# Optimization experiments

Hardware: AMD Instinct MI355X
Metric: run time of the kernel (lower is better)

## Reference

```python
import jax, jax.numpy as jnp
import numpy as np

H = 24
HEAD_DIM = 128
EPS = 1e-6
IP_SCALE = 1.0

def _rms(x, w):
    return x * jax.lax.rsqrt(jnp.mean(x * x, axis=-1, keepdims=True) + EPS) * w

def _heads(x, B):
    # (B, S, H*D) -> (B, H, S, D)
    return x.reshape(B, x.shape[1], H, HEAD_DIM).transpose(0, 2, 1, 3)

def _merge(x):
    B, h, S, d = x.shape
    return x.transpose(0, 2, 1, 3).reshape(B, S, h * d)

def _sdpa(q, k, v):
    s = jnp.einsum('bhqd,bhkd->bhqk', q, k) * (1.0 / np.sqrt(HEAD_DIM))
    return jnp.einsum('bhqk,bhkd->bhqd', jax.nn.softmax(s, axis=-1), v)

def _rope(x, cos, sin):
    # Flux-style real rotary: interleaved pairs, out = x*cos + rot(x)*sin
    xr = x.reshape(x.shape[:-1] + (-1, 2))
    x1, x2 = xr[..., 0], xr[..., 1]
    xrot = jnp.stack([-x2, x1], axis=-1).reshape(x.shape)
    return x * cos + xrot * sin

def setup_inputs():
    key = jax.random.key(0)
    ks = jax.random.split(key, 24)
    B, S_img, L_txt, D, IP_DIM, N_IP = 1, 2048, 512, 3072, 2048, 1024
    S = S_img + L_txt
    def w(k, i, o):
        return jax.random.normal(k, (i, o), jnp.float32) * 0.02
    def b(k, o):
        return jax.random.normal(k, (o,), jnp.float32) * 0.01
    pos = jnp.arange(S, dtype=jnp.float32)
    freqs = 1.0 / (10000.0 ** (jnp.arange(0, HEAD_DIM, 2, dtype=jnp.float32) / HEAD_DIM))
    ang = pos[:, None] * freqs[None, :]
    cos = jnp.repeat(jnp.cos(ang), 2, axis=-1)  # (S, HEAD_DIM)
    sin = jnp.repeat(jnp.sin(ang), 2, axis=-1)
    return {
        'hidden_states': jax.random.normal(ks[0], (B, S_img, D), jnp.float32),
        'encoder_hidden_states': jax.random.normal(ks[1], (B, L_txt, D), jnp.float32),
        'ip_hidden_states': jax.random.normal(ks[2], (B, N_IP, IP_DIM), jnp.float32),
        'rot_cos': cos, 'rot_sin': sin,
        'Wq': w(ks[3], D, D), 'bq': b(ks[4], D),
        'Wk': w(ks[5], D, D), 'bk': b(ks[6], D),
        'Wv': w(ks[7], D, D), 'bv': b(ks[8], D),
        'norm_q_w': jnp.ones((HEAD_DIM,), jnp.float32),
        'norm_k_w': jnp.ones((HEAD_DIM,), jnp.float32),
        'aWq': w(ks[9], D, D), 'abq': b(ks[10], D),
        'aWk': w(ks[11], D, D), 'abk': b(ks[12], D),
        'aWv': w(ks[13], D, D), 'abv': b(ks[14], D),
        'norm_aq_w': jnp.ones((HEAD_DIM,), jnp.float32),
        'norm_ak_w': jnp.ones((HEAD_DIM,), jnp.float32),
        'Wk_ip': w(ks[15], IP_DIM, D), 'bk_ip': b(ks[16], D),
        'Wv_ip': w(ks[17], IP_DIM, D), 'bv_ip': b(ks[18], D),
        'norm_ipq_w': jnp.ones((HEAD_DIM,), jnp.float32),
        'norm_ipk_w': jnp.ones((HEAD_DIM,), jnp.float32),
        'Wo': w(ks[19], D, D), 'bo': b(ks[20], D),
        'Wao': w(ks[21], D, D), 'bao': b(ks[22], D),
    }

def reference(hidden_states, encoder_hidden_states, ip_hidden_states, rot_cos, rot_sin,
              Wq, bq, Wk, bk, Wv, bv, norm_q_w, norm_k_w,
              aWq, abq, aWk, abk, aWv, abv, norm_aq_w, norm_ak_w,
              Wk_ip, bk_ip, Wv_ip, bv_ip, norm_ipq_w, norm_ipk_w,
              Wo, bo, Wao, bao):
    B, S_img, D = hidden_states.shape
    L = encoder_hidden_states.shape[1]
    q = _heads(hidden_states @ Wq + bq, B)   # (B,H,S_img,d)
    k = _heads(hidden_states @ Wk + bk, B)
    v = _heads(hidden_states @ Wv + bv, B)
    # IP-adapter cross-attention: RMS-normed raw image query vs projected image tokens
    ip_q = _rms(q, norm_ipq_w)
    ip_k = _rms(_heads(ip_hidden_states @ Wk_ip + bk_ip, B), norm_ipk_w)
    ip_v = _heads(ip_hidden_states @ Wv_ip + bv_ip, B)
    ip_out = _merge(_sdpa(ip_q, ip_k, ip_v))  # (B, S_img, D)
    # main joint attention with per-head QK RMSNorm
    q = _rms(q, norm_q_w)
    k = _rms(k, norm_k_w)
    eq = _rms(_heads(encoder_hidden_states @ aWq + abq, B), norm_aq_w)
    ek = _rms(_heads(encoder_hidden_states @ aWk + abk, B), norm_ak_w)
    ev = _heads(encoder_hidden_states @ aWv + abv, B)
    q = jnp.concatenate([eq, q], axis=2)
    k = jnp.concatenate([ek, k], axis=2)
    v = jnp.concatenate([ev, v], axis=2)
    q = _rope(q, rot_cos, rot_sin)
    k = _rope(k, rot_cos, rot_sin)
    hs = _merge(_sdpa(q, k, v))  # (B, L+S_img, D)
    enc = hs[:, :L]
    img = hs[:, L:] + IP_SCALE * ip_out
    img = img @ Wo + bo
    enc = enc @ Wao + bao
    return (img, enc)
```

## Files before the change

### kernel.cpp

```cpp
#include <hip/hip_runtime.h>
#include <hip/hip_bf16.h>
#include <cmath>
#include <cstdint>

#define H_    24
#define HD_   128
#define D_    3072
#define SIMG_ 2048
#define LTXT_ 512
#define SALL_ 2560
#define NIP_  1024
#define IPD_  2048

using bf16 = __hip_bfloat16;
typedef __bf16 bf16x8 __attribute__((ext_vector_type(8)));
typedef float  f32x4  __attribute__((ext_vector_type(4)));
typedef short  short8 __attribute__((ext_vector_type(8)));
typedef unsigned int uint4v __attribute__((ext_vector_type(4)));

#define QSCALE_ 0.12751741f

#define SWZ_BLOCK(bx, by)                                              \
  {                                                                    \
    int _gx = gridDim.x;                                               \
    int _hw = blockIdx.x + blockIdx.y * _gx;                           \
    int _n  = _gx * gridDim.y;                                         \
    int _lid = (_hw & 7) * (_n >> 3) + (_hw >> 3);                     \
    bx = _lid % _gx;                                                   \
    by = _lid / _gx;                                                   \
  }

__device__ __forceinline__ unsigned short f2bf(float f) {
  unsigned int u = __float_as_uint(f);
  unsigned int r = (u + 0x7fffu + ((u >> 16) & 1u)) >> 16;
  return (unsigned short)r;
}
__device__ __forceinline__ float bf2f(unsigned short u) {
  return __uint_as_float(((unsigned int)u) << 16);
}
__device__ __forceinline__ unsigned int cvtpk(float lo, float hi) {
  unsigned int pk;
  asm("v_cvt_pk_bf16_f32 %0, %1, %2" : "=v"(pk) : "v"(lo), "v"(hi));
  return pk;
}

__device__ __forceinline__ void gload16(const void* g, void* l) {
  __builtin_amdgcn_global_load_lds(
      (const __attribute__((address_space(1))) unsigned*)g,
      (__attribute__((address_space(3))) unsigned*)l, 16, 0, 0);
}


__global__ void cast_kernel(const float* __restrict__ x, unsigned short* __restrict__ y, int n4) {
  int i = blockIdx.x * blockDim.x + threadIdx.x;
  if (i >= n4) return;
  float4 v = reinterpret_cast<const float4*>(x)[i];
  ushort4 o = make_ushort4(f2bf(v.x), f2bf(v.y), f2bf(v.z), f2bf(v.w));
  reinterpret_cast<ushort4*>(y)[i] = o;
}

__global__ __launch_bounds__(512)
void transpose_cast3_kernel(const float* __restrict__ W0, const float* __restrict__ W1,
                            const float* __restrict__ W2, unsigned short* __restrict__ Wt,
                            int R, int C) {
  __shared__ float tile[64][69];
  const float* W = blockIdx.z == 0 ? W0 : (blockIdx.z == 1 ? W1 : W2);
  unsigned short* dst = Wt + (size_t)blockIdx.z * R * C;
  int bx = blockIdx.x * 64, by = blockIdx.y * 64;
  int tx = threadIdx.x, ty = threadIdx.y;
#pragma unroll
  for (int i = 0; i < 2; i++) {
    int r = ty + 32 * i;
    float4 v = *reinterpret_cast<const float4*>(&W[(size_t)(by + r) * C + bx + tx * 4]);
    tile[r][tx * 4 + 0] = v.x; tile[r][tx * 4 + 1] = v.y;
    tile[r][tx * 4 + 2] = v.z; tile[r][tx * 4 + 3] = v.w;
  }
  __syncthreads();
  int tid = ty * 16 + tx;
  int c = tid >> 3, r0 = (tid & 7) * 8;
  short8 o;
#pragma unroll
  for (int j = 0; j < 8; j++) o[j] = (short)f2bf(tile[r0 + j][c]);
  *reinterpret_cast<short8*>(&dst[(size_t)(bx + c) * R + by + r0]) = o;
}

__device__ __forceinline__ void gemm_core64(const bf16* __restrict__ Ab, const bf16* __restrict__ Bb,
                                            int K, bf16* Alds, bf16* Blds, int t,
                                            int wid, int l16, int lg, f32x4 (&acc)[2][8]) {
  char* AldsB = (char*)Alds + t * 16;
  char* BldsB = (char*)Blds + t * 16;
  for (int kt = 0; kt < K; kt += 64) {
    __syncthreads();
#pragma unroll
    for (int p = 0; p < 4; p++) {
      gload16(Ab + (size_t)(32 * p) * K + kt, AldsB + p * 4096);
      gload16(Bb + (size_t)(32 * p) * K + kt, BldsB + p * 4096);
    }
    __syncthreads();
#pragma unroll
    for (int kb = 0; kb < 2; kb++) {
      bf16x8 af[2], bfr[8];
#pragma unroll
      for (int mi = 0; mi < 2; mi++) {
        int r = wid * 32 + mi * 16 + l16;
        af[mi] = *reinterpret_cast<const bf16x8*>(
            (char*)Alds + r * 128 + ((lg * 16 + kb * 64) ^ ((r & 7) << 4)));
      }
#pragma unroll
      for (int ni = 0; ni < 8; ni++) {
        int r = ni * 16 + l16;
        bfr[ni] = *reinterpret_cast<const bf16x8*>(
            (char*)Blds + r * 128 + ((lg * 16 + kb * 64) ^ ((r & 7) << 4)));
      }
      __builtin_amdgcn_s_setprio(1);
#pragma unroll
      for (int mi = 0; mi < 2; mi++)
#pragma unroll
        for (int ni = 0; ni < 8; ni++)
          acc[mi][ni] = __builtin_amdgcn_mfma_f32_16x16x32_bf16(af[mi], bfr[ni], acc[mi][ni], 0, 0, 0);
      __builtin_amdgcn_s_setprio(0);
    }
  }
}

__global__ __launch_bounds__(256)
void gemm_proj_kernel(const bf16* __restrict__ A, const bf16* __restrict__ Wt,
                      int M, int K, int projmap,
                      const float* __restrict__ b0, const float* __restrict__ b1,
                      const float* __restrict__ b2,
                      const float* __restrict__ rcos, const float* __restrict__ rsin,
                      int pos_off, int tok_off, int Sout,
                      unsigned short* __restrict__ qa_p, const float* __restrict__ nq,
                      unsigned short* __restrict__ ipq_p, const float* __restrict__ nipq, int Sip,
                      unsigned short* __restrict__ ka_p, const float* __restrict__ nk,
                      unsigned short* __restrict__ va_p) {
  __shared__ __align__(16) bf16 Alds[128 * 64];
  __shared__ __align__(16) bf16 Blds[128 * 64];
  bf16* VtS = Alds;
  int t = threadIdx.x;
  int lane = t & 63, wid = t >> 6;
  int l16 = lane & 15, lg = lane >> 4;
  int bx, by;
  SWZ_BLOCK(bx, by);
  int bm = bx * 128;
  int proj = by / 24, head = by % 24;
  int code = (projmap >> (proj * 4)) & 15;
  int arow = t >> 3;
  int aseg = (t & 7) ^ (arow & 7);

  f32x4 acc[2][8];
#pragma unroll
  for (int i = 0; i < 2; i++)
#pragma unroll
    for (int j = 0; j < 8; j++) { acc[i][j][0]=0.f; acc[i][j][1]=0.f; acc[i][j][2]=0.f; acc[i][j][3]=0.f; }

  const bf16* Ab = A  + (size_t)(bm + arow) * K + aseg * 8;
  const bf16* Bb = Wt + (size_t)(by * 128 + arow) * K + aseg * 8;
  gemm_core64(Ab, Bb, K, Alds, Blds, t, wid, l16, lg, acc);

  const float* bias = proj == 0 ? b0 : (proj == 1 ? b1 : b2);
  int bcol = head * 128;

  if (code == 2) {
#pragma unroll
    for (int half = 0; half < 2; half++) {
      __syncthreads();
#pragma unroll
      for (int mi = 0; mi < 2; mi++)
#pragma unroll
        for (int j = 0; j < 4; j++) {
          int tok = wid * 32 + mi * 16 + lg * 4 + j;
#pragma unroll
          for (int ni = 0; ni < 4; ni++) {
            int rc = l16 * 4 + ni;
            float val = acc[mi][ni + 4 * half][j] + bias[bcol + l16 + 16 * (ni + 4 * half)];
            unsigned short uv = f2bf(val);
            VtS[rc * 128 + (tok ^ ((rc & 15) << 3))] = *(bf16*)&uv;
          }
        }
      __syncthreads();
      int rc = t >> 2;
      int tokbase = (t & 3) * 32;
      int s = (rc >> 2) * 8 + (rc & 3) + 4 * half;
#pragma unroll
      for (int it = 0; it < 4; it++) {
        int tok0 = tokbase + it * 8;
        short8 vv = *reinterpret_cast<const short8*>(&VtS[rc * 128 + (tok0 ^ ((rc & 15) << 3))]);
        *reinterpret_cast<short8*>(
            &va_p[((size_t)head * HD_ + s) * Sout + tok_off + bm + tok0]) = vv;
      }
    }
    return;
  }

#pragma unroll
  for (int mi = 0; mi < 2; mi++) {
#pragma unroll
    for (int j = 0; j < 4; j++) {
      int rloc = wid * 32 + mi * 16 + lg * 4 + j;
      int row  = bm + rloc;
      float v[8];
#pragma unroll
      for (int ni = 0; ni < 8; ni++)
        v[ni] = acc[mi][ni][j] + bias[bcol + l16 + 16 * ni];

      float ss = 0.f;
#pragma unroll
      for (int ni = 0; ni < 8; ni++) ss += v[ni] * v[ni];
#pragma unroll
      for (int off = 1; off < 16; off <<= 1) ss += __shfl_xor(ss, off);
      float rr = rsqrtf(ss * (1.f / 128.f) + 1e-6f);

      auto emit = [&](unsigned short* outp, const float* nw, int rope, int scale,
                      int toff, int So) {
        float y[8];
#pragma unroll
        for (int ni = 0; ni < 8; ni++) {
          int col = l16 + 16 * ni;
          y[ni] = v[ni] * rr * nw[col];
        }
        if (rope) {
#pragma unroll
          for (int ni = 0; ni < 8; ni++) {
            int col = l16 + 16 * ni;
            float c  = rcos[(size_t)(pos_off + row) * HD_ + col];
            float sn = rsin[(size_t)(pos_off + row) * HD_ + col];
            float partner = __shfl_xor(y[ni], 1);
            y[ni] = y[ni] * c + ((col & 1) ? partner : -partner) * sn;
          }
        }
        if (scale) {
#pragma unroll
          for (int ni = 0; ni < 8; ni++) y[ni] *= QSCALE_;
        }
        uint4v pk;
        pk[0] = cvtpk(y[0], y[1]); pk[1] = cvtpk(y[2], y[3]);
        pk[2] = cvtpk(y[4], y[5]); pk[3] = cvtpk(y[6], y[7]);
        *reinterpret_cast<uint4v*>(&outp[((size_t)head * So + toff + row) * HD_ + l16 * 8]) = pk;
      };

      if (code == 0) {
        emit(qa_p, nq, 1, 1, tok_off, Sout);
        if (ipq_p) emit(ipq_p, nipq, 0, 1, 0, Sip);
      } else if (code == 1) {
        emit(ka_p, nk, 1, 0, tok_off, Sout);
      } else {
        emit(ka_p, nk, 0, 0, tok_off, Sout);
      }
    }
  }
}

__global__ __launch_bounds__(256)
void gemm_out2_kernel(const bf16* __restrict__ A_img, const bf16* __restrict__ A_enc,
                      const bf16* __restrict__ Wt,
                      const float* __restrict__ bo, const float* __restrict__ bao,
                      float* __restrict__ C_img, float* __restrict__ C_enc) {
  __shared__ __align__(16) bf16 Alds[128 * 64];
  __shared__ __align__(16) bf16 Blds[128 * 64];
  int t = threadIdx.x;
  int lane = t & 63, wid = t >> 6;
  int l16 = lane & 15, lg = lane >> 4;
  int bx, byn;
  SWZ_BLOCK(bx, byn);
  int is_enc = bx >= 16;
  const bf16* A = is_enc ? A_enc : A_img;
  const bf16* W = Wt + (is_enc ? (size_t)D_ * D_ : 0);
  const float* bias = is_enc ? bao : bo;
  float* C = is_enc ? C_enc : C_img;
  int bm = (is_enc ? bx - 16 : bx) * 128;
  int bn = byn * 128;
  int arow = t >> 3;
  int aseg = (t & 7) ^ (arow & 7);
  const int K = D_;

  f32x4 acc[2][8];
#pragma unroll
  for (int i = 0; i < 2; i++)
#pragma unroll
    for (int j = 0; j < 8; j++) { acc[i][j][0]=0.f; acc[i][j][1]=0.f; acc[i][j][2]=0.f; acc[i][j][3]=0.f; }

  const bf16* Ab = A + (size_t)(bm + arow) * K + aseg * 8;
  const bf16* Bb = W + (size_t)(bn + arow) * K + aseg * 8;
  gemm_core64(Ab, Bb, K, Alds, Blds, t, wid, l16, lg, acc);

#pragma unroll
  for (int mi = 0; mi < 2; mi++)
#pragma unroll
    for (int j = 0; j < 4; j++) {
      int row = bm + wid * 32 + mi * 16 + lg * 4 + j;
#pragma unroll
      for (int ni = 0; ni < 8; ni++)
        C[(size_t)row * D_ + bn + l16 + 16 * ni] = acc[mi][ni][j] + bias[bn + l16 + 16 * ni];
    }
}

__global__ __launch_bounds__(256)
void attn_kernel(const bf16* __restrict__ Q1, const bf16* __restrict__ K1,
                 const bf16* __restrict__ Vt1, unsigned short* __restrict__ O1,
                 int Sq1, int Skv1, int nx1,
                 const bf16* __restrict__ Q2, const bf16* __restrict__ K2,
                 const bf16* __restrict__ Vt2, unsigned short* __restrict__ O2,
                 int Sq2, int Skv2) {
  __shared__ __align__(16) bf16 Kl[64 * 128];
  __shared__ __align__(16) bf16 Vl[128 * 64];
  int t = threadIdx.x, lane = t & 63, wid = t >> 6;
  int l16 = lane & 15, lg = lane >> 4;
  int bx, h;
  SWZ_BLOCK(bx, h);
  int is2 = bx >= nx1;
  const bf16* Q  = is2 ? Q2  : Q1;
  const bf16* K  = is2 ? K2  : K1;
  const bf16* Vt = is2 ? Vt2 : Vt1;
  unsigned short* O = is2 ? O2 : O1;
  int Sq  = is2 ? Sq2  : Sq1;
  int Skv = is2 ? Skv2 : Skv1;
  int qb = (is2 ? bx - nx1 : bx) * 128 + wid * 32;

  const bf16* Qh  = Q  + (size_t)h * Sq * HD_;
  const bf16* Kh  = K  + (size_t)h * Skv * HD_;
  const bf16* Vth = Vt + (size_t)h * HD_ * Skv;

  bf16x8 qf[2][4];
#pragma unroll
  for (int m = 0; m < 2; m++)
#pragma unroll
    for (int kb = 0; kb < 4; kb++)
      qf[m][kb] = *reinterpret_cast<const bf16x8*>(
          &Qh[(size_t)(qb + m * 16 + l16) * HD_ + lg * 8 + kb * 32]);

  f32x4 acc[2][8];
#pragma unroll
  for (int m = 0; m < 2; m++)
#pragma unroll
    for (int cb = 0; cb < 8; cb++) { acc[m][cb][0]=0.f; acc[m][cb][1]=0.f; acc[m][cb][2]=0.f; acc[m][cb][3]=0.f; }
  float l_r[2] = {0.f, 0.f};

  int krow = t >> 4;
  int vrow = t >> 3;
  char* KlB = (char*)Kl + t * 16;
  char* VlB = (char*)Vl + t * 16;

  for (int kt = 0; kt < Skv; kt += 64) {
    __syncthreads();
#pragma unroll
    for (int p = 0; p < 4; p++) {
      int rk = p * 16 + krow;
      int sk = (t & 15) ^ (rk & 7);
      gload16(Kh + (size_t)(kt + rk) * HD_ + sk * 8, KlB + p * 4096);
      int rv = p * 32 + vrow;
      int sv = (t & 7) ^ (rv & 7);
      gload16(Vth + (size_t)rv * Skv + kt + sv * 8, VlB + p * 4096);
    }
    __syncthreads();

    f32x4 sc[2][4];
#pragma unroll
    for (int m = 0; m < 2; m++)
#pragma unroll
      for (int nb = 0; nb < 4; nb++) { sc[m][nb][0]=0.f; sc[m][nb][1]=0.f; sc[m][nb][2]=0.f; sc[m][nb][3]=0.f; }
    __builtin_amdgcn_s_setprio(1);
#pragma unroll
    for (int kb = 0; kb < 4; kb++) {
#pragma unroll
      for (int nb = 0; nb < 4; nb++) {
        int r = nb * 16 + l16;
        bf16x8 kf = *reinterpret_cast<const bf16x8*>(
            (char*)Kl + r * 256 + ((lg * 16 + kb * 64) ^ ((r & 7) << 4)));
        sc[0][nb] = __builtin_amdgcn_mfma_f32_16x16x32_bf16(kf, qf[0][kb], sc[0][nb], 0, 0, 0);
        sc[1][nb] = __builtin_amdgcn_mfma_f32_16x16x32_bf16(kf, qf[1][kb], sc[1][nb], 0, 0, 0);
      }
    }
    __builtin_amdgcn_s_setprio(0);
    __syncthreads();

#pragma unroll
    for (int m = 0; m < 2; m++) {
      float part = 0.f;
#pragma unroll
      for (int nb = 0; nb < 4; nb++)
#pragma unroll
        for (int j = 0; j < 4; j++) {
          float p = exp2f(sc[m][nb][j]);
          sc[m][nb][j] = p;
          part += p;
        }
      l_r[m] += part;
      char* Pb = (char*)Kl + (wid * 2 + m) * 2048 + l16 * 128;
#pragma unroll
      for (int nb = 0; nb < 4; nb++) {
#pragma unroll
        for (int w = 0; w < 2; w++) {
          unsigned int pk = cvtpk(sc[m][nb][2 * w], sc[m][nb][2 * w + 1]);
          int colb = nb * 32 + lg * 8 + w * 4;
          *(unsigned int*)(Pb + (colb ^ ((l16 & 7) << 4))) = pk;
        }
      }
    }
    asm volatile("s_waitcnt lgkmcnt(0)" ::: "memory");

#pragma unroll
    for (int kb2 = 0; kb2 < 2; kb2++) {
      bf16x8 pa[2];
#pragma unroll
      for (int m = 0; m < 2; m++)
        pa[m] = *reinterpret_cast<const bf16x8*>(
            (char*)Kl + (wid * 2 + m) * 2048 + l16 * 128 + ((lg * 16 + kb2 * 64) ^ ((l16 & 7) << 4)));
      __builtin_amdgcn_s_setprio(1);
#pragma unroll
      for (int cb = 0; cb < 8; cb++) {
        int d = cb * 16 + l16;
        bf16x8 vf = *reinterpret_cast<const bf16x8*>(
            (char*)Vl + d * 128 + ((lg * 16 + kb2 * 64) ^ ((d & 7) << 4)));
        acc[0][cb] = __builtin_amdgcn_mfma_f32_16x16x32_bf16(pa[0], vf, acc[0][cb], 0, 0, 0);
        acc[1][cb] = __builtin_amdgcn_mfma_f32_16x16x32_bf16(pa[1], vf, acc[1][cb], 0, 0, 0);
      }
      __builtin_amdgcn_s_setprio(0);
    }
  }

#pragma unroll
  for (int m = 0; m < 2; m++) {
    l_r[m] += __shfl_xor(l_r[m], 16);
    l_r[m] += __shfl_xor(l_r[m], 32);
  }

#pragma unroll
  for (int m = 0; m < 2; m++) {
    float inv[4];
#pragma unroll
    for (int j = 0; j < 4; j++) inv[j] = 1.0f / __shfl(l_r[m], lg * 4 + j);
#pragma unroll
    for (int cb = 0; cb < 8; cb++) {
      int col = h * HD_ + (l16 & 7) * 16 + cb * 2 + (l16 >> 3);
#pragma unroll
      for (int j = 0; j < 4; j++) {
        int row = qb + m * 16 + lg * 4 + j;
        O[(size_t)row * (H_ * HD_) + col] = f2bf(acc[m][cb][j] * inv[j]);
      }
    }
  }
}

__global__ void combine_kernel(const unsigned short* __restrict__ attn,
                               const unsigned short* __restrict__ ipo,
                               unsigned short* __restrict__ img_in) {
  size_t i = ((size_t)blockIdx.x * blockDim.x + threadIdx.x) * 8;
  if (i >= (size_t)SIMG_ * D_) return;
  short8 a = *reinterpret_cast<const short8*>(attn + (size_t)LTXT_ * D_ + i);
  short8 b = *reinterpret_cast<const short8*>(ipo + i);
  short8 o;
#pragma unroll
  for (int j = 0; j < 8; j++)
    o[j] = (short)f2bf(bf2f((unsigned short)a[j]) + bf2f((unsigned short)b[j]));
  *reinterpret_cast<short8*>(img_in + i) = o;
}

extern "C" void kernel_launch(void* const* d_in, const int* in_sizes, int n_in,
                              void* d_out, int out_size, void* d_ws, size_t ws_size,
                              hipStream_t stream) {
  const float* hs   = (const float*)d_in[0];
  const float* ehs  = (const float*)d_in[1];
  const float* iphs = (const float*)d_in[2];
  const float* rcos = (const float*)d_in[3];
  const float* rsin = (const float*)d_in[4];
  const float* Wq   = (const float*)d_in[5];  const float* bq   = (const float*)d_in[6];
  const float* Wk   = (const float*)d_in[7];  const float* bk   = (const float*)d_in[8];
  const float* Wv   = (const float*)d_in[9];  const float* bv   = (const float*)d_in[10];
  const float* nqw  = (const float*)d_in[11]; const float* nkw  = (const float*)d_in[12];
  const float* aWq  = (const float*)d_in[13]; const float* abq  = (const float*)d_in[14];
  const float* aWk  = (const float*)d_in[15]; const float* abk  = (const float*)d_in[16];
  const float* aWv  = (const float*)d_in[17]; const float* abv  = (const float*)d_in[18];
  const float* naqw = (const float*)d_in[19]; const float* nakw = (const float*)d_in[20];
  const float* Wkip = (const float*)d_in[21]; const float* bkip = (const float*)d_in[22];
  const float* Wvip = (const float*)d_in[23]; const float* bvip = (const float*)d_in[24];
  const float* nipqw= (const float*)d_in[25]; const float* nipkw= (const float*)d_in[26];
  const float* Wo   = (const float*)d_in[27]; const float* bo   = (const float*)d_in[28];
  const float* Wao  = (const float*)d_in[29]; const float* bao  = (const float*)d_in[30];
  float* out_img = (float*)d_out;
  float* out_enc = out_img + (size_t)SIMG_ * D_;

  char* ws = (char*)d_ws;
  bf16*  Wt      = (bf16*)(ws + 0);
  unsigned short* attn_bf   = (unsigned short*)(ws + 37748736);
  bf16*  qa      = (bf16*)(ws + 56623104);
  bf16*  ka      = (bf16*)(ws + 72351744);
  bf16*  vaT     = (bf16*)(ws + 88080384);
  bf16*  ipq_bf  = (bf16*)(ws + 103809024);
  bf16*  ipk_bf  = (bf16*)(ws + 116391936);
  bf16*  ipvT   = (bf16*)(ws + 122683392);
  bf16*  act_bf  = (bf16*)(ws + 128974848);
  unsigned short* ip_out_bf = (unsigned short*)act_bf;
  bf16*  img_in  = (bf16*)qa;
  if (ws_size < 141557760) return;

  dim3 tb2(16, 32);

  cast_kernel<<<SIMG_ * D_ / 4 / 256, 256, 0, stream>>>(hs, (unsigned short*)act_bf, SIMG_ * D_ / 4);
  transpose_cast3_kernel<<<dim3(48, 48, 3), tb2, 0, stream>>>(Wq, Wk, Wv, (unsigned short*)Wt, D_, D_);
  gemm_proj_kernel<<<dim3(16, 72), 256, 0, stream>>>(act_bf, Wt, SIMG_, D_, 0x210,
      bq, bk, bv, rcos, rsin, LTXT_, LTXT_, SALL_,
      (unsigned short*)qa, nqw, (unsigned short*)ipq_bf, nipqw, SIMG_,
      (unsigned short*)ka, nkw, (unsigned short*)vaT);

  cast_kernel<<<LTXT_ * D_ / 4 / 256, 256, 0, stream>>>(ehs, (unsigned short*)act_bf, LTXT_ * D_ / 4);
  transpose_cast3_kernel<<<dim3(48, 48, 3), tb2, 0, stream>>>(aWq, aWk, aWv, (unsigned short*)Wt, D_, D_);
  gemm_proj_kernel<<<dim3(4, 72), 256, 0, stream>>>(act_bf, Wt, LTXT_, D_, 0x210,
      abq, abk, abv, rcos, rsin, 0, 0, SALL_,
      (unsigned short*)qa, naqw, nullptr, nipqw, SIMG_,
      (unsigned short*)ka, nakw, (unsigned short*)vaT);

  cast_kernel<<<NIP_ * IPD_ / 4 / 256, 256, 0, stream>>>(iphs, (unsigned short*)act_bf, NIP_ * IPD_ / 4);
  transpose_cast3_kernel<<<dim3(48, 32, 2), tb2, 0, stream>>>(Wkip, Wvip, Wvip, (unsigned short*)Wt, IPD_, D_);
  gemm_proj_kernel<<<dim3(8, 48), 256, 0, stream>>>(act_bf, Wt, NIP_, IPD_, 0x23,
      bkip, bvip, bvip, nullptr, nullptr, 0, 0, NIP_,
      nullptr, nullptr, nullptr, nullptr, 0,
      (unsigned short*)ipk_bf, nipkw, (unsigned short*)ipvT);

  transpose_cast3_kernel<<<dim3(48, 48, 2), tb2, 0, stream>>>(Wo, Wao, Wao, (unsigned short*)Wt, D_, D_);

  attn_kernel<<<dim3(SALL_ / 128 + SIMG_ / 128, H_), 256, 0, stream>>>(
      qa, ka, vaT, attn_bf, SALL_, SALL_, SALL_ / 128,
      ipq_bf, ipk_bf, ipvT, ip_out_bf, SIMG_, NIP_);

  combine_kernel<<<SIMG_ * D_ / 8 / 256, 256, 0, stream>>>(attn_bf, ip_out_bf, (unsigned short*)img_in);

  gemm_out2_kernel<<<dim3(20, 24), 256, 0, stream>>>(img_in, (const bf16*)attn_bf, Wt,
                                                     bo, bao, out_img, out_enc);
}
```

Measured before the change: 669.1 us.

## Double-buffer LDS tiles in GEMM and attention kernels to overlap loads with MFMA

Both GEMM kernels and the attention kernel now keep two LDS buffers and issue the global-to-LDS loads for the next K/V or K-tile while the current tile is being multiplied, with one barrier per iteration instead of two. Attention gets a separate per-wave P buffer so it no longer reuses the K tile, and block-to-work mapping is changed to an XCD-aware interleave per attention problem. This doubles LDS use per block, which may reduce occupancy, in exchange for hiding load latency.

```diff
diff --git a/kernel.cpp b/kernel.cpp
--- a/kernel.cpp
+++ b/kernel.cpp
@@ -84,19 +84,26 @@
   *reinterpret_cast<short8*>(&dst[(size_t)(bx + c) * R + by + r0]) = o;
 }
 
-__device__ __forceinline__ void gemm_core64(const bf16* __restrict__ Ab, const bf16* __restrict__ Bb,
-                                            int K, bf16* Alds, bf16* Blds, int t,
-                                            int wid, int l16, int lg, f32x4 (&acc)[2][8]) {
-  char* AldsB = (char*)Alds + t * 16;
-  char* BldsB = (char*)Blds + t * 16;
-  for (int kt = 0; kt < K; kt += 64) {
-    __syncthreads();
+__device__ __forceinline__ void gemm_core64_db(const bf16* __restrict__ Ab,
+                                               const bf16* __restrict__ Bb, int K,
+                                               bf16 (*Alds)[128 * 64], bf16 (*Blds)[128 * 64],
+                                               int t, int wid, int l16, int lg,
+                                               f32x4 (&acc)[2][8]) {
+  auto stage = [&](int b, int kt) {
+    char* AldsB = (char*)Alds[b] + t * 16;
+    char* BldsB = (char*)Blds[b] + t * 16;
 #pragma unroll
     for (int p = 0; p < 4; p++) {
       gload16(Ab + (size_t)(32 * p) * K + kt, AldsB + p * 4096);
       gload16(Bb + (size_t)(32 * p) * K + kt, BldsB + p * 4096);
     }
-    __syncthreads();
+  };
+  int nk = K >> 6;
+  stage(0, 0);
+  __syncthreads();
+  for (int i = 0; i < nk; i++) {
+    int b = i & 1;
+    if (i + 1 < nk) stage(b ^ 1, (i + 1) << 6);
 #pragma unroll
     for (int kb = 0; kb < 2; kb++) {
       bf16x8 af[2], bfr[8];
@@ -104,13 +111,13 @@
       for (int mi = 0; mi < 2; mi++) {
         int r = wid * 32 + mi * 16 + l16;
         af[mi] = *reinterpret_cast<const bf16x8*>(
-            (char*)Alds + r * 128 + ((lg * 16 + kb * 64) ^ ((r & 7) << 4)));
+            (char*)Alds[b] + r * 128 + ((lg * 16 + kb * 64) ^ ((r & 7) << 4)));
       }
 #pragma unroll
       for (int ni = 0; ni < 8; ni++) {
         int r = ni * 16 + l16;
         bfr[ni] = *reinterpret_cast<const bf16x8*>(
-            (char*)Blds + r * 128 + ((lg * 16 + kb * 64) ^ ((r & 7) << 4)));
+            (char*)Blds[b] + r * 128 + ((lg * 16 + kb * 64) ^ ((r & 7) << 4)));
       }
       __builtin_amdgcn_s_setprio(1);
 #pragma unroll
@@ -120,6 +127,7 @@
           acc[mi][ni] = __builtin_amdgcn_mfma_f32_16x16x32_bf16(af[mi], bfr[ni], acc[mi][ni], 0, 0, 0);
       __builtin_amdgcn_s_setprio(0);
     }
+    __syncthreads();
   }
 }
 
@@ -134,9 +142,9 @@
                       unsigned short* __restrict__ ipq_p, const float* __restrict__ nipq, int Sip,
                       unsigned short* __restrict__ ka_p, const float* __restrict__ nk,
                       unsigned short* __restrict__ va_p) {
-  __shared__ __align__(16) bf16 Alds[128 * 64];
-  __shared__ __align__(16) bf16 Blds[128 * 64];
-  bf16* VtS = Alds;
+  __shared__ __align__(16) bf16 Alds[2][128 * 64];
+  __shared__ __align__(16) bf16 Blds[2][128 * 64];
+  bf16* VtS = Alds[0];
   int t = threadIdx.x;
   int lane = t & 63, wid = t >> 6;
   int l16 = lane & 15, lg = lane >> 4;
@@ -156,7 +164,7 @@
 
   const bf16* Ab = A  + (size_t)(bm + arow) * K + aseg * 8;
   const bf16* Bb = Wt + (size_t)(by * 128 + arow) * K + aseg * 8;
-  gemm_core64(Ab, Bb, K, Alds, Blds, t, wid, l16, lg, acc);
+  gemm_core64_db(Ab, Bb, K, Alds, Blds, t, wid, l16, lg, acc);
 
   const float* bias = proj == 0 ? b0 : (proj == 1 ? b1 : b2);
   int bcol = head * 128;
@@ -256,8 +264,8 @@
                       const bf16* __restrict__ Wt,
                       const float* __restrict__ bo, const float* __restrict__ bao,
                       float* __restrict__ C_img, float* __restrict__ C_enc) {
-  __shared__ __align__(16) bf16 Alds[128 * 64];
-  __shared__ __align__(16) bf16 Blds[128 * 64];
+  __shared__ __align__(16) bf16 Alds[2][128 * 64];
+  __shared__ __align__(16) bf16 Blds[2][128 * 64];
   int t = threadIdx.x;
   int lane = t & 63, wid = t >> 6;
   int l16 = lane & 15, lg = lane >> 4;
@@ -282,7 +290,7 @@
 
   const bf16* Ab = A + (size_t)(bm + arow) * K + aseg * 8;
   const bf16* Bb = W + (size_t)(bn + arow) * K + aseg * 8;
-  gemm_core64(Ab, Bb, K, Alds, Blds, t, wid, l16, lg, acc);
+  gemm_core64_db(Ab, Bb, K, Alds, Blds, t, wid, l16, lg, acc);
 
 #pragma unroll
   for (int mi = 0; mi < 2; mi++)
@@ -302,20 +310,31 @@
                  const bf16* __restrict__ Q2, const bf16* __restrict__ K2,
                  const bf16* __restrict__ Vt2, unsigned short* __restrict__ O2,
                  int Sq2, int Skv2) {
-  __shared__ __align__(16) bf16 Kl[64 * 128];
-  __shared__ __align__(16) bf16 Vl[128 * 64];
+  __shared__ __align__(16) bf16 Kl[2][64 * 128];
+  __shared__ __align__(16) bf16 Vl[2][128 * 64];
+  __shared__ __align__(16) bf16 Pl[4][2][16 * 64];
   int t = threadIdx.x, lane = t & 63, wid = t >> 6;
   int l16 = lane & 15, lg = lane >> 4;
-  int bx, h;
-  SWZ_BLOCK(bx, h);
-  int is2 = bx >= nx1;
+
+  int hw = blockIdx.x + blockIdx.y * gridDim.x;
+  int n1 = nx1 * 24;
+  int is2, bx, h;
+  if (hw < n1) {
+    int lid = (hw & 7) * (n1 >> 3) + (hw >> 3);
+    bx = lid % nx1; h = lid / nx1; is2 = 0;
+  } else {
+    int hw2 = hw - n1;
+    int n2 = gridDim.x * gridDim.y - n1;
+    int lid = (hw2 & 7) * (n2 >> 3) + (hw2 >> 3);
+    bx = lid % 16; h = lid / 16; is2 = 1;
+  }
   const bf16* Q  = is2 ? Q2  : Q1;
   const bf16* K  = is2 ? K2  : K1;
   const bf16* Vt = is2 ? Vt2 : Vt1;
   unsigned short* O = is2 ? O2 : O1;
   int Sq  = is2 ? Sq2  : Sq1;
   int Skv = is2 ? Skv2 : Skv1;
-  int qb = (is2 ? bx - nx1 : bx) * 128 + wid * 32;
+  int qb = bx * 128 + wid * 32;
 
   const bf16* Qh  = Q  + (size_t)h * Sq * HD_;
   const bf16* Kh  = K  + (size_t)h * Skv * HD_;
@@ -336,23 +355,27 @@
     for (int cb = 0; cb < 8; cb++) { acc[m][cb][0]=0.f; acc[m][cb][1]=0.f; acc[m][cb][2]=0.f; acc[m][cb][3]=0.f; }
   float l_r[2] = {0.f, 0.f};
 
-  int krow = t >> 4;
-  int vrow = t >> 3;
-  char* KlB = (char*)Kl + t * 16;
-  char* VlB = (char*)Vl + t * 16;
-
-  for (int kt = 0; kt < Skv; kt += 64) {
-    __syncthreads();
+  auto STAGE = [&](int b, int kt) {
+    char* KlB = (char*)Kl[b] + t * 16;
+    char* VlB = (char*)Vl[b] + t * 16;
 #pragma unroll
     for (int p = 0; p < 4; p++) {
-      int rk = p * 16 + krow;
+      int rk = p * 16 + (t >> 4);
       int sk = (t & 15) ^ (rk & 7);
       gload16(Kh + (size_t)(kt + rk) * HD_ + sk * 8, KlB + p * 4096);
-      int rv = p * 32 + vrow;
+      int rv = p * 32 + (t >> 3);
       int sv = (t & 7) ^ (rv & 7);
       gload16(Vth + (size_t)rv * Skv + kt + sv * 8, VlB + p * 4096);
     }
-    __syncthreads();
+  };
+
+  int nt = Skv >> 6;
+  STAGE(0, 0);
+  __syncthreads();
+
+  for (int ti = 0; ti < nt; ti++) {
+    int b = ti & 1;
+    if (ti + 1 < nt) STAGE(b ^ 1, (ti + 1) * 64);
 
     f32x4 sc[2][4];
 #pragma unroll
@@ -366,13 +389,12 @@
       for (int nb = 0; nb < 4; nb++) {
         int r = nb * 16 + l16;
         bf16x8 kf = *reinterpret_cast<const bf16x8*>(
-            (char*)Kl + r * 256 + ((lg * 16 + kb * 64) ^ ((r & 7) << 4)));
+            (char*)Kl[b] + r * 256 + ((lg * 16 + kb * 64) ^ ((r & 7) << 4)));
         sc[0][nb] = __builtin_amdgcn_mfma_f32_16x16x32_bf16(kf, qf[0][kb], sc[0][nb], 0, 0, 0);
         sc[1][nb] = __builtin_amdgcn_mfma_f32_16x16x32_bf16(kf, qf[1][kb], sc[1][nb], 0, 0, 0);
       }
     }
     __builtin_amdgcn_s_setprio(0);
-    __syncthreads();
 
 #pragma unroll
     for (int m = 0; m < 2; m++) {
@@ -386,7 +408,7 @@
           part += p;
         }
       l_r[m] += part;
-      char* Pb = (char*)Kl + (wid * 2 + m) * 2048 + l16 * 128;
+      char* Pb = (char*)&Pl[wid][m][0] + l16 * 128;
 #pragma unroll
       for (int nb = 0; nb < 4; nb++) {
 #pragma unroll
@@ -405,18 +427,19 @@
 #pragma unroll
       for (int m = 0; m < 2; m++)
         pa[m] = *reinterpret_cast<const bf16x8*>(
-            (char*)Kl + (wid * 2 + m) * 2048 + l16 * 128 + ((lg * 16 + kb2 * 64) ^ ((l16 & 7) << 4)));
+            (char*)&Pl[wid][m][0] + l16 * 128 + ((lg * 16 + kb2 * 64) ^ ((l16 & 7) << 4)));
       __builtin_amdgcn_s_setprio(1);
 #pragma unroll
       for (int cb = 0; cb < 8; cb++) {
         int d = cb * 16 + l16;
         bf16x8 vf = *reinterpret_cast<const bf16x8*>(
-            (char*)Vl + d * 128 + ((lg * 16 + kb2 * 64) ^ ((d & 7) << 4)));
+            (char*)Vl[b] + d * 128 + ((lg * 16 + kb2 * 64) ^ ((d & 7) << 4)));
         acc[0][cb] = __builtin_amdgcn_mfma_f32_16x16x32_bf16(pa[0], vf, acc[0][cb], 0, 0, 0);
         acc[1][cb] = __builtin_amdgcn_mfma_f32_16x16x32_bf16(pa[1], vf, acc[1][cb], 0, 0, 0);
       }
       __builtin_amdgcn_s_setprio(0);
     }
+    __syncthreads();
   }
 
 #pragma unroll
```

After: 614.0 us. 1.09x faster.
